# Performance work log

Measured on AMD Instinct MI355X. Metric: run time of the kernel, lower is better.

Reference implementation:

```python
import jax, jax.numpy as jnp
import numpy as np


def setup_inputs() -> dict:
    key = jax.random.key(0)
    k0, k1, k2, k3 = jax.random.split(key, 4)
    B, H, W, C, h = 2, 64, 64, 256, 8
    N = H * W
    # per-pixel, per-head (dy, dx) match offsets; a few pixels of displacement
    max_offset = jax.random.normal(k0, (B, N, h, 2), dtype=jnp.float32) * 4.0
    q = jax.random.normal(k1, (B, N, C), dtype=jnp.float32)
    k = jax.random.normal(k2, (B, N, C), dtype=jnp.float32)
    v = jax.random.normal(k3, (B, N, C), dtype=jnp.float32)
    return {"max_offset": max_offset, "q": q, "k": k, "v": v,
            "H": H, "W": W, "r_h": 3, "r_w": 3}


def reference(max_offset, q, k, v, H, W, r_h, r_w):
    """MatchAttention fused forward (l1_norm, scale=1.0).

    Each query pixel (y,x), head g attends to a (2*r_h+1)x(2*r_w+1) window
    centered at (y,x) + round(max_offset[...,g]), clamped to the image.
    Similarity is the negative L1 distance between q and gathered k.
    Returns (output [B,N,C], attn_out [B,N,h,K]).
    """
    B, N, C = q.shape
    h = max_offset.shape[2]
    Ch = C // h
    scale = 1.0
    attn_type = "l1_norm"  # fixed; 'l2_norm' would use squared distance

    # window deltas, K = (2*r_h+1)*(2*r_w+1)
    dy = jnp.arange(-r_h, r_h + 1)
    dx = jnp.arange(-r_w, r_w + 1)
    gy, gx = jnp.meshgrid(dy, dx, indexing="ij")
    ddy, ddx = gy.reshape(-1), gx.reshape(-1)  # [K]

    ys = (jnp.arange(N) // W)[None, :, None]  # [1,N,1]
    xs = (jnp.arange(N) % W)[None, :, None]

    off = jnp.round(max_offset).astype(jnp.int32)  # [B,N,h,2] (dy,dx)
    cy = ys + off[..., 0]                          # [B,N,h] window center
    cx = xs + off[..., 1]
    py = jnp.clip(cy[..., None] + ddy, 0, H - 1)   # [B,N,h,K]
    px = jnp.clip(cx[..., None] + ddx, 0, W - 1)
    idx = py * W + px                              # flat pixel index, [B,N,h,K]

    # split heads and move head axis forward: [B,h,N,Ch]
    qh = q.reshape(B, N, h, Ch).transpose(0, 2, 1, 3)
    kh = k.reshape(B, N, h, Ch).transpose(0, 2, 1, 3)
    vh = v.reshape(B, N, h, Ch).transpose(0, 2, 1, 3)
    idx_t = idx.transpose(0, 2, 1, 3)              # [B,h,N,K]

    # gather windows: [B,h,N,K,Ch]
    gather = jax.vmap(jax.vmap(lambda tbl, i: tbl[i]))
    kg = gather(kh, idx_t)
    vg = gather(vh, idx_t)

    # negative L1 distance similarity, softmax over window
    sim = -scale * jnp.abs(qh[:, :, :, None, :] - kg).sum(-1)  # [B,h,N,K]
    attn = jax.nn.softmax(sim, axis=-1)

    out = jnp.einsum("bhnk,bhnkc->bhnc", attn, vg)
    output = out.transpose(0, 2, 1, 3).reshape(B, N, C)
    attn_out = attn.transpose(0, 2, 1, 3)          # [B,N,h,K]
    return output, attn_out
```

## Files before the change

kernel.cpp:

```cpp
#include <hip/hip_runtime.h>
#include <math.h>

constexpr int B = 2, H = 64, W = 64, C = 256, NH = 8, CH = 32;
constexpr int R = 3, KW = 7, KK = 49, N = H * W;
constexpr int ECH = 4;
constexpr int PIX = 32;

__global__ void __launch_bounds__(256) match_attn_kernel(
    const float* __restrict__ moff, const float* __restrict__ qp,
    const float* __restrict__ kp, const float* __restrict__ vp,
    float* __restrict__ outp, float* __restrict__ attnp) {
  __shared__ __align__(16) float part4[PIX][KK][4];
  __shared__ __align__(16) float wbuf[PIX][52];

  const int t = threadIdx.x;
  const int e8 = t & 7;
  const int p = t >> 3;

  const int xcd = blockIdx.x & 7;
  const int rest = blockIdx.x >> 3;
  const int bg = xcd * 2 + (rest >> 7);
  const int slot = rest & 127;
  const int y = slot >> 1;
  const int x = (slot & 1) * PIX + p;
  const int g = bg & 7;
  const int b = bg >> 3;
  const int n = y * W + x;

  const float2 off = *(const float2*)(moff + ((size_t)(b * N + n) * NH + g) * 2);
  const int cy = y + (int)rintf(off.x);
  const int cx = x + (int)rintf(off.y);

  const int chn = g * CH + e8 * ECH;
  const float4 q0 = *(const float4*)(qp + (size_t)(b * N + n) * C + chn);
  const float* kb = kp + (size_t)b * N * C + chn;
  const float* vb = vp + (size_t)b * N * C + chn;

  for (int iy = 0; iy < KW; ++iy) {
    const int py = min(max(cy + iy - R, 0), H - 1);
    const float* krow = kb + (size_t)(py * W) * C;
#pragma unroll
    for (int ix = 0; ix < KW; ++ix) {
      const int px = min(max(cx + ix - R, 0), W - 1);
      const float4 k0 = *(const float4*)(krow + (size_t)px * C);
      float s = fabsf(q0.x - k0.x) + fabsf(q0.y - k0.y) +
                fabsf(q0.z - k0.z) + fabsf(q0.w - k0.w);
      s += __shfl_xor(s, 1);
      if ((e8 & 1) == 0) part4[p][iy * KW + ix][e8 >> 1] = s;
    }
  }
  __syncthreads();

  float ev[7];
  float d = 0.f;
#pragma unroll
  for (int j = 0; j < 7; ++j) {
    const int kk = e8 + 8 * j;
    if (kk < KK) {
      const float4 pa = *(const float4*)&part4[p][kk][0];
      const float e = __expf(-(pa.x + pa.y + pa.z + pa.w));
      ev[j] = e;
      d += e;
    }
  }
  d += __shfl_xor(d, 1);
  d += __shfl_xor(d, 2);
  d += __shfl_xor(d, 4);
  const float inv = 1.0f / d;

  float* attn_px = attnp + ((size_t)(b * N + n) * NH + g) * KK;
#pragma unroll
  for (int j = 0; j < 7; ++j) {
    const int kk = e8 + 8 * j;
    if (kk < KK) {
      const float w = ev[j] * inv;
      wbuf[p][kk] = w;
      attn_px[kk] = w;
    }
  }
  __syncthreads();

  float4 acc = {0.f, 0.f, 0.f, 0.f};
  for (int iy = 0; iy < KW; ++iy) {
    const int py = min(max(cy + iy - R, 0), H - 1);
    const float* vrow = vb + (size_t)(py * W) * C;
#pragma unroll
    for (int ix = 0; ix < KW; ++ix) {
      const int px = min(max(cx + ix - R, 0), W - 1);
      const float4 v0 = *(const float4*)(vrow + (size_t)px * C);
      const float w = wbuf[p][iy * KW + ix];
      acc.x += w * v0.x; acc.y += w * v0.y;
      acc.z += w * v0.z; acc.w += w * v0.w;
    }
  }
  *(float4*)(outp + (size_t)(b * N + n) * C + chn) = acc;
}

extern "C" void kernel_launch(void* const* d_in, const int* in_sizes, int n_in,
                              void* d_out, int out_size, void* d_ws, size_t ws_size,
                              hipStream_t stream) {
  const float* moff = (const float*)d_in[0];
  const float* q    = (const float*)d_in[1];
  const float* k    = (const float*)d_in[2];
  const float* v    = (const float*)d_in[3];
  float* out  = (float*)d_out;
  float* attn = out + (size_t)B * N * C;

  const int grid = B * NH * N / PIX;
  match_attn_kernel<<<grid, 256, 0, stream>>>(moff, q, k, v, out, attn);
}
```

Measured before the change: 123.8 us.

## Replace LDS partial sums and barriers with DPP reductions and shuffles

Reduces the per-window L1 partial sums across the 8 channel lanes with DPP moves and computes exponentials and the softmax denominator inline, eliminating the shared-memory staging buffers and both block barriers. Attention weights are kept in registers and broadcast to the value-gather loop with wave shuffles. Clamped window coordinates are precomputed as byte offsets to cut address arithmetic. Every lane now computes the exp for every window position, and register-array dynamic indexing may spill if the outer loop isn't unrolled.

```diff
diff --git a/kernel.cpp b/kernel.cpp
--- a/kernel.cpp
+++ b/kernel.cpp
@@ -3,19 +3,27 @@
 
 constexpr int B = 2, H = 64, W = 64, C = 256, NH = 8, CH = 32;
 constexpr int R = 3, KW = 7, KK = 49, N = H * W;
-constexpr int ECH = 4;
 constexpr int PIX = 32;
+
+template <int CTRL>
+static __device__ __forceinline__ float dpp_mov(float v) {
+  union { float f; int i; } u;
+  u.f = v;
+  u.i = __builtin_amdgcn_update_dpp(u.i, u.i, CTRL, 0xf, 0xf, true);
+  return u.f;
+}
+#define DPP_QUAD_XOR1 0xB1
+#define DPP_QUAD_XOR2 0x4E
+#define DPP_HALF_MIRROR 0x141
 
 __global__ void __launch_bounds__(256) match_attn_kernel(
     const float* __restrict__ moff, const float* __restrict__ qp,
     const float* __restrict__ kp, const float* __restrict__ vp,
     float* __restrict__ outp, float* __restrict__ attnp) {
-  __shared__ __align__(16) float part4[PIX][KK][4];
-  __shared__ __align__(16) float wbuf[PIX][52];
-
   const int t = threadIdx.x;
   const int e8 = t & 7;
   const int p = t >> 3;
+  const int lbase = (t & 63) & ~7;
 
   const int xcd = blockIdx.x & 7;
   const int rest = blockIdx.x >> 3;
@@ -31,64 +39,58 @@
   const int cy = y + (int)rintf(off.x);
   const int cx = x + (int)rintf(off.y);
 
-  const int chn = g * CH + e8 * ECH;
+  int pxo[KW], pyo[KW];
+#pragma unroll
+  for (int i = 0; i < KW; ++i) {
+    pxo[i] = min(max(cx + i - R, 0), W - 1) << 10;
+    pyo[i] = min(max(cy + i - R, 0), H - 1) * (W << 10);
+  }
+  const int chn = g * CH + e8 * 4;
+  const int cb = chn * 4;
+  const char* kimg = (const char*)(kp + (size_t)b * N * C);
+  const char* vimg = (const char*)(vp + (size_t)b * N * C);
+
   const float4 q0 = *(const float4*)(qp + (size_t)(b * N + n) * C + chn);
-  const float* kb = kp + (size_t)b * N * C + chn;
-  const float* vb = vp + (size_t)b * N * C + chn;
 
+  float ev[7];
+#pragma unroll
+  for (int j = 0; j < 7; ++j) ev[j] = 0.f;
+  float d = 0.f;
   for (int iy = 0; iy < KW; ++iy) {
-    const int py = min(max(cy + iy - R, 0), H - 1);
-    const float* krow = kb + (size_t)(py * W) * C;
+    const int rowo = cb + pyo[iy];
 #pragma unroll
     for (int ix = 0; ix < KW; ++ix) {
-      const int px = min(max(cx + ix - R, 0), W - 1);
-      const float4 k0 = *(const float4*)(krow + (size_t)px * C);
+      const float4 k0 = *(const float4*)(kimg + (rowo + pxo[ix]));
       float s = fabsf(q0.x - k0.x) + fabsf(q0.y - k0.y) +
                 fabsf(q0.z - k0.z) + fabsf(q0.w - k0.w);
-      s += __shfl_xor(s, 1);
-      if ((e8 & 1) == 0) part4[p][iy * KW + ix][e8 >> 1] = s;
+      s += dpp_mov<DPP_QUAD_XOR1>(s);
+      s += dpp_mov<DPP_QUAD_XOR2>(s);
+      s += dpp_mov<DPP_HALF_MIRROR>(s);
+      const float e = __expf(-s);
+      d += e;
+      const int kk = iy * KW + ix;
+      if ((kk & 7) == e8) ev[kk >> 3] = e;
     }
   }
-  __syncthreads();
-
-  float ev[7];
-  float d = 0.f;
-#pragma unroll
-  for (int j = 0; j < 7; ++j) {
-    const int kk = e8 + 8 * j;
-    if (kk < KK) {
-      const float4 pa = *(const float4*)&part4[p][kk][0];
-      const float e = __expf(-(pa.x + pa.y + pa.z + pa.w));
-      ev[j] = e;
-      d += e;
-    }
-  }
-  d += __shfl_xor(d, 1);
-  d += __shfl_xor(d, 2);
-  d += __shfl_xor(d, 4);
   const float inv = 1.0f / d;
 
   float* attn_px = attnp + ((size_t)(b * N + n) * NH + g) * KK;
 #pragma unroll
   for (int j = 0; j < 7; ++j) {
-    const int kk = e8 + 8 * j;
-    if (kk < KK) {
-      const float w = ev[j] * inv;
-      wbuf[p][kk] = w;
-      attn_px[kk] = w;
-    }
+    const int kk = 8 * j + e8;
+    const float w = ev[j] * inv;
+    ev[j] = w;
+    if (kk < KK) attn_px[kk] = w;
   }
-  __syncthreads();
 
   float4 acc = {0.f, 0.f, 0.f, 0.f};
   for (int iy = 0; iy < KW; ++iy) {
-    const int py = min(max(cy + iy - R, 0), H - 1);
-    const float* vrow = vb + (size_t)(py * W) * C;
+    const int rowo = cb + pyo[iy];
 #pragma unroll
     for (int ix = 0; ix < KW; ++ix) {
-      const int px = min(max(cx + ix - R, 0), W - 1);
-      const float4 v0 = *(const float4*)(vrow + (size_t)px * C);
-      const float w = wbuf[p][iy * KW + ix];
+      const int kk = iy * KW + ix;
+      const float w = __shfl(ev[kk >> 3], lbase | (kk & 7), 64);
+      const float4 v0 = *(const float4*)(vimg + (rowo + pxo[ix]));
       acc.x += w * v0.x; acc.y += w * v0.y;
       acc.z += w * v0.z; acc.w += w * v0.w;
     }
```

Result: slower. 127.5 us (+2.9%).
